# Optimization experiments

Hardware: AMD Instinct MI355X
Metric: run time of the kernel (lower is better)

Reference implementation:

```python
import jax, jax.numpy as jnp
import numpy as np

D_MODEL = 1024
N_HEADS = 16
HEAD_DIM = D_MODEL // N_HEADS


def setup_inputs() -> dict:
    key = jax.random.key(0)
    k1, k2, k3 = jax.random.split(key, 3)
    scale = 1.0 / np.sqrt(D_MODEL)
    x = jax.random.normal(k1, (4, 2048, D_MODEL), dtype=jnp.float32)
    w_qkv = jax.random.normal(k2, (D_MODEL, 3 * D_MODEL), dtype=jnp.float32) * scale
    b_qkv = jnp.zeros((3 * D_MODEL,), dtype=jnp.float32)
    w_proj = jax.random.normal(k3, (D_MODEL, D_MODEL), dtype=jnp.float32) * scale
    b_proj = jnp.zeros((D_MODEL,), dtype=jnp.float32)
    return {"x": x, "w_qkv": w_qkv, "b_qkv": b_qkv, "w_proj": w_proj, "b_proj": b_proj}


def reference(x, w_qkv, b_qkv, w_proj, b_proj):
    B, T, C = x.shape
    H, Dh = N_HEADS, HEAD_DIM
    qkv = x @ w_qkv + b_qkv                       # (B, T, 3C)
    qkv = qkv.reshape(B, T, 3, H, Dh)
    q = qkv[:, :, 0].transpose(0, 2, 1, 3)        # (B, H, T, Dh)
    k = qkv[:, :, 1].transpose(0, 2, 1, 3)
    v = qkv[:, :, 2].transpose(0, 2, 1, 3)
    att = jnp.einsum('bhqd,bhkd->bhqk', q, k) / jnp.sqrt(jnp.float32(Dh))
    causal = jnp.tril(jnp.ones((T, T), dtype=bool))
    att = jnp.where(causal[None, None], att, -jnp.inf)
    att = jax.nn.softmax(att, axis=-1)
    y = jnp.einsum('bhqk,bhkd->bhqd', att, v)     # (B, H, T, Dh)
    y = y.transpose(0, 2, 1, 3).reshape(B, T, C)
    return y @ w_proj + b_proj
```

## Files before the change

kernel.cpp:

```cpp
#include <hip/hip_runtime.h>
#include <hip/hip_bf16.h>
#include <math.h>

typedef __bf16 bf16_t;
typedef __bf16 bf16x4 __attribute__((ext_vector_type(4)));
typedef __bf16 bf16x8 __attribute__((ext_vector_type(8)));
typedef float floatx4 __attribute__((ext_vector_type(4)));

#define AS1 __attribute__((address_space(1)))
#define AS3 __attribute__((address_space(3)))

__device__ bf16_t g_xb[8192 * 1024];
__device__ bf16_t g_wqkvT[3072 * 1024];
__device__ bf16_t g_wprojT[1024 * 1024];
__device__ float  g_bqkv[3072];
__device__ float  g_bproj[1024];
__device__ bf16_t g_qkv[3ull * 64 * 2048 * 64];
#define HBREG (64ull * 2048 * 64)

__global__ __launch_bounds__(256) void cvt_x(const float* __restrict__ src,
                                             const float* __restrict__ bq,
                                             const float* __restrict__ bp) {
  int blk = blockIdx.x;
  int tid = threadIdx.x;
  if (blk < 4096) {
    int i0 = (blk * 256 + tid) * 8;
    const float4* s = (const float4*)src;
    float4 a = s[i0 / 4], b = s[i0 / 4 + 1];
    bf16x8 v;
    v[0] = (bf16_t)a.x; v[1] = (bf16_t)a.y; v[2] = (bf16_t)a.z; v[3] = (bf16_t)a.w;
    v[4] = (bf16_t)b.x; v[5] = (bf16_t)b.y; v[6] = (bf16_t)b.z; v[7] = (bf16_t)b.w;
    *(bf16x8*)&g_xb[i0] = v;
  } else if (blk == 4096) {
    for (int i = tid; i < 3072; i += 256) g_bqkv[i] = bq[i];
  } else {
    for (int i = tid; i < 1024; i += 256) g_bproj[i] = bp[i];
  }
}

__global__ __launch_bounds__(256) void tr64(const float* __restrict__ wqkv,
                                            const float* __restrict__ wproj) {
  __shared__ bf16_t tile[64][65];
  const int R = 1024;
  int bx = blockIdx.x;
  const float* in;
  bf16_t* out;
  int C, c0;
  if (bx < 48) { in = wqkv; out = g_wqkvT; C = 3072; c0 = bx * 64; }
  else         { in = wproj; out = g_wprojT; C = 1024; c0 = (bx - 48) * 64; }
  int r0 = blockIdx.y * 64;
  int tid = threadIdx.x;
#pragma unroll
  for (int it = 0; it < 16; ++it) {
    int idx = tid + it * 256;
    int r = idx >> 6, c = idx & 63;
    tile[r][c] = (bf16_t)in[(size_t)(r0 + r) * C + (c0 + c)];
  }
  __syncthreads();
#pragma unroll
  for (int it = 0; it < 16; ++it) {
    int idx = tid + it * 256;
    int r = idx >> 6, c = idx & 63;
    out[(size_t)(c0 + r) * R + (r0 + c)] = tile[c][r];
  }
}

__global__ __launch_bounds__(256) void gemm_bt(float* __restrict__ out_ext,
                                               int M, int N, int K,
                                               int amode, int bsel, int cmode) {
  __shared__ bf16_t As[2][128 * 32];
  __shared__ bf16_t Bs[2][128 * 32];
  const bf16_t* A = (amode == 0) ? g_xb : g_qkv;
  const bf16_t* Bt = bsel ? g_wprojT : g_wqkvT;
  const float* bias = bsel ? g_bproj : g_bqkv;
  const int tid = threadIdx.x;
  const int m0 = blockIdx.y * 128, n0 = blockIdx.x * 128;
  const int lane = tid & 63, wave = tid >> 6;
  const int wm = wave >> 1, wn = wave & 1;
  const int quad = lane >> 4, l16 = lane & 15;
  const int wub = tid & ~63;

  floatx4 acc[4][4] = {};

  for (int k0 = 0; k0 < K; k0 += 64) {
#pragma unroll
    for (int sl = 0; sl < 2; ++sl) {
      int kk0 = k0 + sl * 32;
#pragma unroll
      for (int it = 0; it < 2; ++it) {
        int idx = tid + it * 256;
        int row = idx >> 2;
        int c8 = (idx & 3) * 8;
        int wbase = (it * 256 + wub) * 8;
        const bf16_t* asrc;
        if (amode == 0) {
          asrc = &A[(size_t)(m0 + row) * K + kk0 + c8];
        } else {
          int m = m0 + row;
          int b = m >> 11, t = m & 2047;
          int h = kk0 >> 6, dd = (kk0 & 63) + c8;
          asrc = &A[((size_t)((b * 16 + h) * 2048 + t)) * 64 + dd];
        }
        const bf16_t* bsrc = &Bt[(size_t)(n0 + row) * K + kk0 + c8];
        __builtin_amdgcn_global_load_lds((const AS1 void*)asrc,
                                         (AS3 void*)&As[sl][wbase], 16, 0, 0);
        __builtin_amdgcn_global_load_lds((const AS1 void*)bsrc,
                                         (AS3 void*)&Bs[sl][wbase], 16, 0, 0);
      }
    }
    __syncthreads();
#pragma unroll
    for (int sl = 0; sl < 2; ++sl) {
      bf16x8 af[4], bfr[4];
#pragma unroll
      for (int t = 0; t < 4; ++t) {
        af[t] = *(const bf16x8*)&As[sl][(wm * 64 + t * 16 + l16) * 32 + quad * 8];
        bfr[t] = *(const bf16x8*)&Bs[sl][(wn * 64 + t * 16 + l16) * 32 + quad * 8];
      }
#pragma unroll
      for (int tm = 0; tm < 4; ++tm)
#pragma unroll
        for (int tn = 0; tn < 4; ++tn)
          acc[tm][tn] = __builtin_amdgcn_mfma_f32_16x16x32_bf16(
              af[tm], bfr[tn], acc[tm][tn], 0, 0, 0);
    }
    __syncthreads();
  }

#pragma unroll
  for (int tm = 0; tm < 4; ++tm) {
#pragma unroll
    for (int tn = 0; tn < 4; ++tn) {
      int ncol = n0 + wn * 64 + tn * 16 + l16;
      float bb = bias[ncol];
      int mbase = m0 + wm * 64 + tm * 16 + quad * 4;
      if (cmode == 0) {
        int which = ncol >> 10;
        int h = (ncol >> 6) & 15;
        int d = ncol & 63;
        int b = mbase >> 11, t = mbase & 2047;
        if (which == 2) {
          bf16x4 pk;
#pragma unroll
          for (int r = 0; r < 4; ++r) pk[r] = (bf16_t)(acc[tm][tn][r] + bb);
          size_t dst = 2 * HBREG + ((size_t)((b * 16 + h) * 64 + d)) * 2048 + t;
          *(bf16x4*)&g_qkv[dst] = pk;
        } else {
          size_t base = (size_t)which * HBREG +
                        ((size_t)((b * 16 + h) * 2048 + t)) * 64 + d;
#pragma unroll
          for (int r = 0; r < 4; ++r)
            g_qkv[base + (size_t)r * 64] = (bf16_t)(acc[tm][tn][r] + bb);
        }
      } else {
#pragma unroll
        for (int r = 0; r < 4; ++r)
          out_ext[(size_t)(mbase + r) * N + ncol] = acc[tm][tn][r] + bb;
      }
    }
  }
}

__global__ __launch_bounds__(256) void attn64() {
  const int LDW = 72;
  __shared__ bf16_t Qs[64 * 72];
  __shared__ bf16_t Ks[64 * 72];
  __shared__ bf16_t Vt[64 * 72];
  bf16_t* Ps = Qs;
  const float C1 = 0.1803368801111204f;
  const float C2 = -23.083120654223414f;
  const int tid = threadIdx.x;
  const int qpair = blockIdx.x;
  const int bh = blockIdx.y;
  const bf16_t* Qb  = g_qkv + (size_t)bh * 2048 * 64;
  const bf16_t* Kb  = g_qkv + HBREG + (size_t)bh * 2048 * 64;
  const bf16_t* VTb = g_qkv + 2 * HBREG + (size_t)bh * 64 * 2048;
  bf16_t* Yb = g_qkv + (size_t)bh * 2048 * 64;
  const int lane = tid & 63, wave = tid >> 6;
  const int quad = lane >> 4, l16 = lane & 15;
  const int row0 = tid >> 3, c80 = (tid & 7) * 8;

  bf16x8 ones8;
#pragma unroll
  for (int j = 0; j < 8; ++j) ones8[j] = (bf16_t)1.0f;

  for (int ph = 0; ph < 2; ++ph) {
    const int qi = ph ? (31 - qpair) : qpair;
    const int q0 = qi * 64;

    *(bf16x8*)&Qs[row0 * LDW + c80] =
        *(const bf16x8*)&Qb[(size_t)(q0 + row0) * 64 + c80];
    *(bf16x8*)&Qs[(row0 + 32) * LDW + c80] =
        *(const bf16x8*)&Qb[(size_t)(q0 + row0 + 32) * 64 + c80];
    __syncthreads();
    bf16x8 aq0 = *(const bf16x8*)&Qs[(wave * 16 + l16) * LDW + quad * 8];
    bf16x8 aq1 = *(const bf16x8*)&Qs[(wave * 16 + l16) * LDW + 32 + quad * 8];

    floatx4 o[4] = {};
    floatx4 osum = {};

    bf16x8 kp0 = *(const bf16x8*)&Kb[(size_t)row0 * 64 + c80];
    bf16x8 kp1 = *(const bf16x8*)&Kb[(size_t)(row0 + 32) * 64 + c80];
    bf16x8 vp0 = *(const bf16x8*)&VTb[(size_t)row0 * 2048 + c80];
    bf16x8 vp1 = *(const bf16x8*)&VTb[(size_t)(row0 + 32) * 2048 + c80];

    const int ntiles = qi + 1;
    for (int kt = 0; kt < ntiles; ++kt) {
      __syncthreads();
      *(bf16x8*)&Ks[row0 * LDW + c80] = kp0;
      *(bf16x8*)&Ks[(row0 + 32) * LDW + c80] = kp1;
      *(bf16x8*)&Vt[row0 * LDW + c80] = vp0;
      *(bf16x8*)&Vt[(row0 + 32) * LDW + c80] = vp1;
      if (kt + 1 < ntiles) {
        const int k1 = (kt + 1) * 64;
        kp0 = *(const bf16x8*)&Kb[(size_t)(k1 + row0) * 64 + c80];
        kp1 = *(const bf16x8*)&Kb[(size_t)(k1 + row0 + 32) * 64 + c80];
        vp0 = *(const bf16x8*)&VTb[(size_t)row0 * 2048 + k1 + c80];
        vp1 = *(const bf16x8*)&VTb[(size_t)(row0 + 32) * 2048 + k1 + c80];
      }
      __syncthreads();

      const int k0 = kt * 64;
      floatx4 s[4];
#pragma unroll
      for (int tn = 0; tn < 4; ++tn) {
        bf16x8 bk0 = *(const bf16x8*)&Ks[(tn * 16 + l16) * LDW + quad * 8];
        bf16x8 bk1 = *(const bf16x8*)&Ks[(tn * 16 + l16) * LDW + 32 + quad * 8];
        floatx4 z = {};
        z = __builtin_amdgcn_mfma_f32_16x16x32_bf16(aq0, bk0, z, 0, 0, 0);
        z = __builtin_amdgcn_mfma_f32_16x16x32_bf16(aq1, bk1, z, 0, 0, 0);
        s[tn] = z;
      }

      if (kt == qi) {
#pragma unroll
        for (int tn = 0; tn < 4; ++tn) {
          int kcol = k0 + tn * 16 + l16;
#pragma unroll
          for (int r = 0; r < 4; ++r) {
            int qrow = q0 + wave * 16 + quad * 4 + r;
            float p = exp2f(fminf(fmaf(s[tn][r], C1, C2), 30.f));
            s[tn][r] = (kcol > qrow) ? 0.f : p;
          }
        }
      } else {
#pragma unroll
        for (int tn = 0; tn < 4; ++tn)
#pragma unroll
          for (int r = 0; r < 4; ++r)
            s[tn][r] = exp2f(fminf(fmaf(s[tn][r], C1, C2), 30.f));
      }

      bf16_t* Pw = &Ps[wave * 16 * LDW];
#pragma unroll
      for (int tn = 0; tn < 4; ++tn)
#pragma unroll
        for (int r = 0; r < 4; ++r)
          Pw[(quad * 4 + r) * LDW + tn * 16 + l16] = (bf16_t)s[tn][r];

      bf16x8 ap0 = *(const bf16x8*)&Pw[l16 * LDW + quad * 8];
      bf16x8 ap1 = *(const bf16x8*)&Pw[l16 * LDW + 32 + quad * 8];
#pragma unroll
      for (int tn = 0; tn < 4; ++tn) {
        bf16x8 bv0 = *(const bf16x8*)&Vt[(tn * 16 + l16) * LDW + quad * 8];
        bf16x8 bv1 = *(const bf16x8*)&Vt[(tn * 16 + l16) * LDW + 32 + quad * 8];
        o[tn] = __builtin_amdgcn_mfma_f32_16x16x32_bf16(ap0, bv0, o[tn], 0, 0, 0);
        o[tn] = __builtin_amdgcn_mfma_f32_16x16x32_bf16(ap1, bv1, o[tn], 0, 0, 0);
      }
      osum = __builtin_amdgcn_mfma_f32_16x16x32_bf16(ap0, ones8, osum, 0, 0, 0);
      osum = __builtin_amdgcn_mfma_f32_16x16x32_bf16(ap1, ones8, osum, 0, 0, 0);
    }

#pragma unroll
    for (int tn = 0; tn < 4; ++tn) {
      int d = tn * 16 + l16;
#pragma unroll
      for (int r = 0; r < 4; ++r) {
        int t = q0 + wave * 16 + quad * 4 + r;
        float v = o[tn][r] / osum[r];
        Yb[(size_t)t * 64 + d] = (bf16_t)v;
      }
    }
    __syncthreads();
  }
}

extern "C" void kernel_launch(void* const* d_in, const int* in_sizes, int n_in,
                              void* d_out, int out_size, void* d_ws, size_t ws_size,
                              hipStream_t stream) {
  const float* x      = (const float*)d_in[0];
  const float* w_qkv  = (const float*)d_in[1];
  const float* b_qkv  = (const float*)d_in[2];
  const float* w_proj = (const float*)d_in[3];
  const float* b_proj = (const float*)d_in[4];
  (void)d_ws; (void)ws_size;

  cvt_x<<<4098, 256, 0, stream>>>(x, b_qkv, b_proj);
  tr64<<<dim3(64, 16), 256, 0, stream>>>(w_qkv, w_proj);

  gemm_bt<<<dim3(24, 64), 256, 0, stream>>>(nullptr, 8192, 3072, 1024, 0, 0, 0);

  attn64<<<dim3(16, 64), 256, 0, stream>>>();

  gemm_bt<<<dim3(8, 64), 256, 0, stream>>>((float*)d_out, 8192, 1024, 1024, 1, 1, 1);
}
```

Measured before the change: 318.1 us.

## Replace GEMM with 256x128 tiled, double-buffered, swizzled-LDS pipelined kernel

```diff
diff --git a/kernel.cpp b/kernel.cpp
--- a/kernel.cpp
+++ b/kernel.cpp
@@ -6,6 +6,7 @@
 typedef __bf16 bf16x4 __attribute__((ext_vector_type(4)));
 typedef __bf16 bf16x8 __attribute__((ext_vector_type(8)));
 typedef float floatx4 __attribute__((ext_vector_type(4)));
+typedef unsigned int u32;
 
 #define AS1 __attribute__((address_space(1)))
 #define AS3 __attribute__((address_space(3)))
@@ -65,97 +66,202 @@
   }
 }
 
-__global__ __launch_bounds__(256) void gemm_bt(float* __restrict__ out_ext,
+#define MFMA16(a, b, c) __builtin_amdgcn_mfma_f32_16x16x32_bf16(a, b, c, 0, 0, 0)
+#define SB0() __builtin_amdgcn_sched_barrier(0)
+#define PH_MID()                                          \
+  do {                                                    \
+    SB0();                                                \
+    __builtin_amdgcn_s_barrier();                         \
+    SB0();                                                \
+    asm volatile("s_waitcnt lgkmcnt(0)" ::: "memory");    \
+    SB0();                                                \
+  } while (0)
+#define PH_END()                                          \
+  do {                                                    \
+    SB0();                                                \
+    __builtin_amdgcn_s_barrier();                         \
+    SB0();                                                \
+  } while (0)
+
+__global__ __launch_bounds__(512) void gemm256(float* __restrict__ out_ext,
                                                int M, int N, int K,
                                                int amode, int bsel, int cmode) {
-  __shared__ bf16_t As[2][128 * 32];
-  __shared__ bf16_t Bs[2][128 * 32];
-  const bf16_t* A = (amode == 0) ? g_xb : g_qkv;
+  __shared__ alignas(16) bf16_t As[2][2][256 * 32];
+  __shared__ alignas(16) bf16_t Bs[2][2][128 * 32];
+  (void)M;
+  const bf16_t* Ag = (amode == 0) ? g_xb : g_qkv;
   const bf16_t* Bt = bsel ? g_wprojT : g_wqkvT;
   const float* bias = bsel ? g_bproj : g_bqkv;
   const int tid = threadIdx.x;
-  const int m0 = blockIdx.y * 128, n0 = blockIdx.x * 128;
+
+  int gx = gridDim.x;
+  int nwg = gx * gridDim.y;
+  int lin = blockIdx.y * gx + blockIdx.x;
+  int swz = (lin & 7) * (nwg >> 3) + (lin >> 3);
+  int bx = swz % gx, by = swz / gx;
+  const int m0 = by * 256, n0 = bx * 128;
+
   const int lane = tid & 63, wave = tid >> 6;
   const int wm = wave >> 1, wn = wave & 1;
   const int quad = lane >> 4, l16 = lane & 15;
-  const int wub = tid & ~63;
+
+  u32 L0 = (u32)tid * 16u, L1 = (u32)(tid + 512) * 16u;
+  u32 y0 = L0 ^ (((L0 >> 7) & 3u) << 4);
+  u32 y1 = L1 ^ (((L1 >> 7) & 3u) << 4);
+  int ar0 = y0 >> 6, ac0 = (y0 & 63) >> 1;
+  int ar1 = y1 >> 6, ac1 = (y1 & 63) >> 1;
+  u32 a_go0, a_go1, ktstride;
+  if (amode == 0) {
+    a_go0 = (u32)(m0 + ar0) * (u32)K + (u32)ac0;
+    a_go1 = (u32)(m0 + ar1) * (u32)K + (u32)ac1;
+    ktstride = 64u;
+  } else {
+    int mA = m0 + ar0, bb_ = mA >> 11, tt = mA & 2047;
+    a_go0 = (u32)bb_ * 2097152u + (u32)tt * 64u + (u32)ac0;
+    mA = m0 + ar1; bb_ = mA >> 11; tt = mA & 2047;
+    a_go1 = (u32)bb_ * 2097152u + (u32)tt * 64u + (u32)ac1;
+    ktstride = 131072u;
+  }
+  u32 b_go = (u32)(n0 + ar0) * (u32)K + (u32)ac0;
+
+  auto stageA = [&](int kt_, int s_) {
+    int bb = kt_ & 1;
+    const bf16_t* s0 = Ag + (size_t)(a_go0 + (u32)kt_ * ktstride + (u32)s_ * 32u);
+    const bf16_t* s1 = Ag + (size_t)(a_go1 + (u32)kt_ * ktstride + (u32)s_ * 32u);
+    __builtin_amdgcn_global_load_lds((const AS1 void*)s0,
+                                     (AS3 void*)&As[bb][s_][(u32)tid * 8u], 16, 0, 0);
+    __builtin_amdgcn_global_load_lds((const AS1 void*)s1,
+                                     (AS3 void*)&As[bb][s_][(u32)(tid + 512) * 8u], 16, 0, 0);
+  };
+  auto stageB = [&](int kt_, int s_) {
+    int bb = kt_ & 1;
+    const bf16_t* s0 = Bt + (size_t)(b_go + (u32)kt_ * 64u + (u32)s_ * 32u);
+    __builtin_amdgcn_global_load_lds((const AS1 void*)s0,
+                                     (AS3 void*)&Bs[bb][s_][(u32)tid * 8u], 16, 0, 0);
+  };
+
+  int saB[4], sbB[4];
+#pragma unroll
+  for (int i = 0; i < 4; ++i) {
+    u32 xa = (u32)(wm * 64 + i * 16 + l16) * 64u + (u32)quad * 16u;
+    saB[i] = (int)(xa ^ (((xa >> 7) & 3u) << 4));
+    u32 xb = (u32)(wn * 64 + i * 16 + l16) * 64u + (u32)quad * 16u;
+    sbB[i] = (int)(xb ^ (((xb >> 7) & 3u) << 4));
+  }
 
   floatx4 acc[4][4] = {};
-
-  for (int k0 = 0; k0 < K; k0 += 64) {
-#pragma unroll
-    for (int sl = 0; sl < 2; ++sl) {
-      int kk0 = k0 + sl * 32;
-#pragma unroll
-      for (int it = 0; it < 2; ++it) {
-        int idx = tid + it * 256;
-        int row = idx >> 2;
-        int c8 = (idx & 3) * 8;
-        int wbase = (it * 256 + wub) * 8;
-        const bf16_t* asrc;
-        if (amode == 0) {
-          asrc = &A[(size_t)(m0 + row) * K + kk0 + c8];
-        } else {
-          int m = m0 + row;
-          int b = m >> 11, t = m & 2047;
-          int h = kk0 >> 6, dd = (kk0 & 63) + c8;
-          asrc = &A[((size_t)((b * 16 + h) * 2048 + t)) * 64 + dd];
-        }
-        const bf16_t* bsrc = &Bt[(size_t)(n0 + row) * K + kk0 + c8];
-        __builtin_amdgcn_global_load_lds((const AS1 void*)asrc,
-                                         (AS3 void*)&As[sl][wbase], 16, 0, 0);
-        __builtin_amdgcn_global_load_lds((const AS1 void*)bsrc,
-                                         (AS3 void*)&Bs[sl][wbase], 16, 0, 0);
-      }
-    }
-    __syncthreads();
-#pragma unroll
-    for (int sl = 0; sl < 2; ++sl) {
-      bf16x8 af[4], bfr[4];
-#pragma unroll
-      for (int t = 0; t < 4; ++t) {
-        af[t] = *(const bf16x8*)&As[sl][(wm * 64 + t * 16 + l16) * 32 + quad * 8];
-        bfr[t] = *(const bf16x8*)&Bs[sl][(wn * 64 + t * 16 + l16) * 32 + quad * 8];
-      }
-#pragma unroll
-      for (int tm = 0; tm < 4; ++tm)
-#pragma unroll
-        for (int tn = 0; tn < 4; ++tn)
-          acc[tm][tn] = __builtin_amdgcn_mfma_f32_16x16x32_bf16(
-              af[tm], bfr[tn], acc[tm][tn], 0, 0, 0);
-    }
-    __syncthreads();
-  }
-
-#pragma unroll
-  for (int tm = 0; tm < 4; ++tm) {
-#pragma unroll
-    for (int tn = 0; tn < 4; ++tn) {
-      int ncol = n0 + wn * 64 + tn * 16 + l16;
+  const int NT = K >> 6;
+
+  stageA(0, 0); SB0(); stageB(0, 0); SB0();
+  stageA(0, 1); SB0(); stageB(0, 1); SB0();
+  stageA(1, 0); SB0(); stageB(1, 0); SB0();
+  asm volatile("s_waitcnt vmcnt(6)" ::: "memory");
+  __builtin_amdgcn_s_barrier();
+  SB0();
+
+  for (int kt = 0; kt < NT; ++kt) {
+    const int b = kt & 1;
+    const char* Ab0 = (const char*)&As[b][0][0];
+    const char* Ab1 = (const char*)&As[b][1][0];
+    const char* Bb0 = (const char*)&Bs[b][0][0];
+    const char* Bb1 = (const char*)&Bs[b][1][0];
+    bf16x8 a0[4], bf2[2];
+
+#pragma unroll
+    for (int i = 0; i < 4; ++i) a0[i] = *(const bf16x8*)(Ab0 + saB[i]);
+    bf2[0] = *(const bf16x8*)(Bb0 + sbB[0]);
+    bf2[1] = *(const bf16x8*)(Bb0 + sbB[1]);
+    if (kt + 1 < NT) stageA(kt + 1, 1);
+    PH_MID();
+    __builtin_amdgcn_s_setprio(1);
+#pragma unroll
+    for (int i = 0; i < 4; ++i) {
+      acc[i][0] = MFMA16(a0[i], bf2[0], acc[i][0]);
+      acc[i][1] = MFMA16(a0[i], bf2[1], acc[i][1]);
+    }
+    __builtin_amdgcn_s_setprio(0);
+    PH_END();
+
+    bf2[0] = *(const bf16x8*)(Bb0 + sbB[2]);
+    bf2[1] = *(const bf16x8*)(Bb0 + sbB[3]);
+    if (kt + 1 < NT) stageB(kt + 1, 1);
+    PH_MID();
+    __builtin_amdgcn_s_setprio(1);
+#pragma unroll
+    for (int i = 0; i < 4; ++i) {
+      acc[i][2] = MFMA16(a0[i], bf2[0], acc[i][2]);
+      acc[i][3] = MFMA16(a0[i], bf2[1], acc[i][3]);
+    }
+    __builtin_amdgcn_s_setprio(0);
+    SB0();
+    if (kt + 1 < NT) asm volatile("s_waitcnt vmcnt(6)" ::: "memory");
+    else             asm volatile("s_waitcnt vmcnt(0)" ::: "memory");
+    __builtin_amdgcn_s_barrier();
+    SB0();
+
+#pragma unroll
+    for (int i = 0; i < 4; ++i) a0[i] = *(const bf16x8*)(Ab1 + saB[i]);
+    bf2[0] = *(const bf16x8*)(Bb1 + sbB[0]);
+    bf2[1] = *(const bf16x8*)(Bb1 + sbB[1]);
+    if (kt + 2 < NT) stageA(kt + 2, 0);
+    PH_MID();
+    __builtin_amdgcn_s_setprio(1);
+#pragma unroll
+    for (int i = 0; i < 4; ++i) {
+      acc[i][0] = MFMA16(a0[i], bf2[0], acc[i][0]);
+      acc[i][1] = MFMA16(a0[i], bf2[1], acc[i][1]);
+    }
+    __builtin_amdgcn_s_setprio(0);
+    PH_END();
+
+    bf2[0] = *(const bf16x8*)(Bb1 + sbB[2]);
+    bf2[1] = *(const bf16x8*)(Bb1 + sbB[3]);
+    if (kt + 2 < NT) stageB(kt + 2, 0);
+    PH_MID();
+    __builtin_amdgcn_s_setprio(1);
+#pragma unroll
+    for (int i = 0; i < 4; ++i) {
+      acc[i][2] = MFMA16(a0[i], bf2[0], acc[i][2]);
+      acc[i][3] = MFMA16(a0[i], bf2[1], acc[i][3]);
+    }
+    __builtin_amdgcn_s_setprio(0);
+    SB0();
+    if (kt + 2 < NT)      asm volatile("s_waitcnt vmcnt(6)" ::: "memory");
+    else if (kt + 1 < NT) asm volatile("s_waitcnt vmcnt(3)" ::: "memory");
+    else                  asm volatile("s_waitcnt vmcnt(0)" ::: "memory");
+    __builtin_amdgcn_s_barrier();
+    SB0();
+  }
+
+#pragma unroll
+  for (int mf = 0; mf < 4; ++mf) {
+#pragma unroll
+    for (int nf = 0; nf < 4; ++nf) {
+      int ncol = n0 + wn * 64 + nf * 16 + l16;
       float bb = bias[ncol];
-      int mbase = m0 + wm * 64 + tm * 16 + quad * 4;
+      int mbase = m0 + wm * 64 + mf * 16 + quad * 4;
       if (cmode == 0) {
         int which = ncol >> 10;
         int h = (ncol >> 6) & 15;
         int d = ncol & 63;
-        int b = mbase >> 11, t = mbase & 2047;
+        int b_ = mbase >> 11, t = mbase & 2047;
         if (which == 2) {
           bf16x4 pk;
 #pragma unroll
-          for (int r = 0; r < 4; ++r) pk[r] = (bf16_t)(acc[tm][tn][r] + bb);
-          size_t dst = 2 * HBREG + ((size_t)((b * 16 + h) * 64 + d)) * 2048 + t;
+          for (int r = 0; r < 4; ++r) pk[r] = (bf16_t)(acc[mf][nf][r] + bb);
+          size_t dst = 2 * HBREG + ((size_t)((b_ * 16 + h) * 64 + d)) * 2048 + t;
           *(bf16x4*)&g_qkv[dst] = pk;
         } else {
           size_t base = (size_t)which * HBREG +
-                        ((size_t)((b * 16 + h) * 2048 + t)) * 64 + d;
+                        ((size_t)((b_ * 16 + h) * 2048 + t)) * 64 + d;
 #pragma unroll
           for (int r = 0; r < 4; ++r)
-            g_qkv[base + (size_t)r * 64] = (bf16_t)(acc[tm][tn][r] + bb);
+            g_qkv[base + (size_t)r * 64] = (bf16_t)(acc[mf][nf][r] + bb);
         }
       } else {
 #pragma unroll
         for (int r = 0; r < 4; ++r)
-          out_ext[(size_t)(mbase + r) * N + ncol] = acc[tm][tn][r] + bb;
+          out_ext[(size_t)(mbase + r) * N + ncol] = acc[mf][nf][r] + bb;
       }
     }
   }
@@ -298,9 +404,9 @@
   cvt_x<<<4098, 256, 0, stream>>>(x, b_qkv, b_proj);
   tr64<<<dim3(64, 16), 256, 0, stream>>>(w_qkv, w_proj);
 
-  gemm_bt<<<dim3(24, 64), 256, 0, stream>>>(nullptr, 8192, 3072, 1024, 0, 0, 0);
+  gemm256<<<dim3(24, 32), 512, 0, stream>>>(nullptr, 8192, 3072, 1024, 0, 0, 0);
 
   attn64<<<dim3(16, 64), 256, 0, stream>>>();
 
-  gemm_bt<<<dim3(8, 64), 256, 0, stream>>>((float*)d_out, 8192, 1024, 1024, 1, 1, 1);
+  gemm256<<<dim3(8, 32), 512, 0, stream>>>((float*)d_out, 8192, 1024, 1024, 1, 1, 1);
 }
```

Result: no change. 322.3 us (+1.3%).
